# Optimization experiments

Measured on AMD Instinct MI355X. Metric: run time of the kernel, lower is better.

## Reference

```python
import jax, jax.numpy as jnp
import numpy as np

SIGMA = 1.0
DELTA = 1.0
TOPK = 10
TOPK_HALF = 5  # int(np.around(TOPK / 2))


def l2norm(x):
    # F.normalize: x / max(||x||, 1e-12)
    n = jnp.linalg.norm(x, axis=-1, keepdims=True)
    return x / jnp.maximum(n, 1e-12)


def cdist(a, b):
    # pairwise euclidean distance with grad-safe sqrt (0 on exact-zero dists)
    d2 = (jnp.sum(a * a, axis=1)[:, None] + jnp.sum(b * b, axis=1)[None, :]
          - 2.0 * a @ b.T)
    d2 = jnp.maximum(d2, 0.0)
    return jnp.where(d2 > 0.0, jnp.sqrt(jnp.where(d2 > 0.0, d2, 1.0)), 0.0)


def rc_weights(t_emb, idx):
    # all of this is under torch.no_grad() in the original
    N = t_emb.shape[0]
    T_dist = cdist(t_emb, t_emb)
    W_P = jnp.exp(-(T_dist ** 2) / SIGMA)
    same_id = idx[:, None] == idx[None, :]
    W_P_copy = jnp.where(same_id, 1.0, W_P)
    _, topk_index = jax.lax.top_k(W_P_copy, TOPK)            # [N, k]
    topk_half_index = topk_index[:, :TOPK_HALF]               # [N, k/2]
    rows = jnp.arange(N)[:, None]
    W_NN = jnp.zeros((N, N), W_P.dtype).at[rows, topk_index].set(1.0)
    V = (((W_NN + W_NN.T) / 2.0) == 1.0).astype(W_P.dtype)    # mutual-NN graph
    # vectorized form of the per-row loop:
    # W_C_tilda[i, j] = V[i, j] * |N(i) \cap N(j)| / |N(i)|
    deg = V.sum(axis=1)                                       # |N(i)| per row
    VV = V @ V                                                # V symmetric -> (V@V)[i,j] = |N(i) cap N(j)|
    W_C_tilda = jnp.where(V > 0.0, VV / jnp.maximum(deg, 1.0)[:, None], 0.0)
    W_C_hat = W_C_tilda[topk_half_index].mean(axis=1)         # [N, N]
    W_C = (W_C_hat + W_C_hat.T) / 2.0
    W = (W_P + W_C) / 2.0
    off_diag = 1.0 - jnp.eye(N, dtype=W.dtype)
    pos_weight = W * off_diag
    neg_weight = (1.0 - W) * off_diag
    return pos_weight, neg_weight


def rc_loss(s_emb, t_emb, idx):
    s_emb = l2norm(s_emb)        # disable_mu=True
    t_emb = l2norm(t_emb)
    N = s_emb.shape[0]
    S_dist = cdist(s_emb, s_emb)
    S_dist = S_dist / S_dist.mean(axis=1, keepdims=True)
    pos_w, neg_w = rc_weights(t_emb, idx)
    pos_w = jax.lax.stop_gradient(pos_w)
    neg_w = jax.lax.stop_gradient(neg_w)
    pull = jax.nn.relu(S_dist) ** 2 * pos_w
    push = jax.nn.relu(DELTA - S_dist) ** 2 * neg_w
    return (pull.sum() + push.sum()) / (N * (N - 1))


def kl_loss(s_f, s_g):
    # disable_mu=True -> normalize both
    s_f = l2norm(s_f)
    s_g = l2norm(s_g)
    N = s_f.shape[0]
    S_dist = cdist(s_f, s_f)
    S_dist = S_dist / S_dist.mean(axis=1, keepdims=True)
    S_bg = cdist(s_g, s_g)
    S_bg = S_bg / S_bg.mean(axis=1, keepdims=True)
    log_q = jax.nn.log_softmax(-S_dist, axis=-1)
    log_p = jax.nn.log_softmax(jax.lax.stop_gradient(-S_bg), axis=-1)
    p = jnp.exp(log_p)
    return jnp.sum(p * (log_p - log_q)) / N


def setup_inputs() -> dict:
    key = jax.random.key(0)
    k1, k2, k3, k4 = jax.random.split(key, 4)
    N = 4096
    s_f = jax.random.normal(k1, (N, 512), jnp.float32)
    s_g = jax.random.normal(k2, (N, 512), jnp.float32)
    t_g = jax.random.normal(k3, (N, 1024), jnp.float32)
    idx = jax.random.randint(k4, (N,), 0, 2048, jnp.int64 if jax.config.jax_enable_x64 else jnp.int32)
    return {"s_f": s_f, "s_g": s_g, "t_g": t_g, "idx": idx}


def reference(s_f, s_g, t_g, idx):
    loss_RC_f = rc_loss(s_f, t_g, idx)
    loss_RC_g = rc_loss(s_g, t_g, idx)
    loss_RC = (loss_RC_f + loss_RC_g) / 2.0
    loss_KL = kl_loss(s_f, s_g)
    return loss_RC, loss_KL, loss_RC + loss_KL
```

## Files before the change

### kernel.cpp

```cpp
#include <hip/hip_runtime.h>
#include <hip/hip_bf16.h>

#define NN 4096
typedef unsigned short u16;
typedef __bf16 bf16x8 __attribute__((ext_vector_type(8)));
typedef float f32x4 __attribute__((ext_vector_type(4)));
typedef u16 u16x8 __attribute__((ext_vector_type(8)));

typedef const __attribute__((address_space(1))) void* gptr_t;
typedef __attribute__((address_space(3))) void* lptr_t;

__device__ inline u16 bf16bits(float v) {
    __bf16 h = (__bf16)v;
    return __builtin_bit_cast(u16, h);
}
__device__ inline float bf16val(float v) {
    __bf16 h = (__bf16)v;
    return (float)h;
}
__device__ inline float b2f(u16 b) { return __uint_as_float(((unsigned)b) << 16); }

__device__ inline float block_sum(float v, volatile float* sbuf) {
    int lane = threadIdx.x & 63, wv = threadIdx.x >> 6;
#pragma unroll
    for (int o = 32; o > 0; o >>= 1) v += __shfl_xor(v, o, 64);
    if (lane == 0) sbuf[wv] = v;
    __syncthreads();
    float r = sbuf[0] + sbuf[1] + sbuf[2] + sbuf[3];
    __syncthreads();
    return r;
}

template <int D>
__global__ void normalize_kernel(const float* __restrict__ in, u16* __restrict__ outb,
                                 float* __restrict__ ssout) {
    __shared__ float sbuf[4];
    constexpr int NV = D / 4;
    int row = blockIdx.x, tid = threadIdx.x;
    const float4* x4 = (const float4*)(in + (size_t)row * D);
    float4 v = make_float4(0.f, 0.f, 0.f, 0.f);
    if (tid < NV) v = x4[tid];
    float s = v.x * v.x + v.y * v.y + v.z * v.z + v.w * v.w;
    float tot = block_sum(s, sbuf);
    float inv = 1.0f / fmaxf(sqrtf(tot), 1e-12f);
    float sb = 0.f;
    if (tid < NV) {
        float b0 = bf16val(v.x * inv), b1 = bf16val(v.y * inv);
        float b2 = bf16val(v.z * inv), b3 = bf16val(v.w * inv);
        ushort4 o;
        o.x = bf16bits(v.x * inv);
        o.y = bf16bits(v.y * inv);
        o.z = bf16bits(v.z * inv);
        o.w = bf16bits(v.w * inv);
        ((ushort4*)(outb + (size_t)row * D))[tid] = o;
        sb = b0 * b0 + b1 * b1 + b2 * b2 + b3 * b3;
    }
    float totb = block_sum(sb, sbuf);
    if (tid == 0) ssout[row] = totb;
}

#define TS 132
__launch_bounds__(256)
__global__ void gram_merged(const u16* __restrict__ tb, const u16* __restrict__ fb,
                            const u16* __restrict__ gb, const float* __restrict__ ss_t,
                            const float* __restrict__ ss_f, const float* __restrict__ ss_g,
                            u16* __restrict__ WP, u16* __restrict__ Sf, u16* __restrict__ Sg,
                            float* __restrict__ rsf, float* __restrict__ rsg) {
    __shared__ __align__(16) u16 smem[24576];

    int bid = blockIdx.x;
    int seg = (bid < 528) ? 0 : (bid < 1056 ? 1 : 2);
    int p = bid - seg * 528;
    int l = (p & 7) * 66 + (p >> 3);
    int by = 0, rem = l;
    while (rem >= 32 - by) { rem -= 32 - by; ++by; }
    int bx = by + rem;

    const u16* X = (seg == 0) ? tb : (seg == 1 ? fb : gb);
    const float* ss = (seg == 0) ? ss_t : (seg == 1 ? ss_f : ss_g);
    u16* outp = (seg == 0) ? WP : (seg == 1 ? Sf : Sg);
    float* rowsum = (seg == 0) ? nullptr : (seg == 1 ? rsf : rsg);
    const int K = (seg == 0) ? 1024 : 512;
    const bool mode1 = (seg != 0);
    const bool offdiag = (bx != by);

    const int tid = threadIdx.x;
    const int wv = tid >> 6, lane = tid & 63;
    const int wr = wv >> 1, wc = wv & 1;
    const int brow = by * 128, bcol = bx * 128;
    const int r = lane & 15, kc = lane >> 4;
    const int crow = lane >> 2;
    const int koff = (lane & 3) * 8;

    f32x4 acc[4][4];
#pragma unroll
    for (int mi = 0; mi < 4; ++mi)
#pragma unroll
        for (int ni = 0; ni < 4; ++ni) acc[mi][ni] = (f32x4){0.f, 0.f, 0.f, 0.f};

    auto STAGE = [&](int buf, int k0) {
#pragma unroll
        for (int cc = 0; cc < 2; ++cc) {
            int c = wv * 2 + cc;
            const u16* ga = X + (size_t)(brow + c * 16 + crow) * K + k0 + koff;
            const u16* gbp = X + (size_t)(bcol + c * 16 + crow) * K + k0 + koff;
            __builtin_amdgcn_global_load_lds((gptr_t)ga, (lptr_t)&smem[buf * 4096 + c * 512], 16, 0, 0);
            __builtin_amdgcn_global_load_lds((gptr_t)gbp, (lptr_t)&smem[12288 + buf * 4096 + c * 512], 16, 0, 0);
        }
    };

    const int NT = K / 32;
    STAGE(0, 0);
    STAGE(1, 32);
    for (int t = 0; t < NT; ++t) {
        int cur = t % 3;
        if (t == NT - 1) asm volatile("s_waitcnt vmcnt(0)" ::: "memory");
        else             asm volatile("s_waitcnt vmcnt(4)" ::: "memory");
        __builtin_amdgcn_sched_barrier(0);
        __builtin_amdgcn_s_barrier();

        bf16x8 af[4], bfr[4];
#pragma unroll
        for (int mi = 0; mi < 4; ++mi)
            af[mi] = *(const bf16x8*)&smem[cur * 4096 + (wr * 64 + mi * 16 + r) * 32 + kc * 8];
#pragma unroll
        for (int ni = 0; ni < 4; ++ni)
            bfr[ni] = *(const bf16x8*)&smem[12288 + cur * 4096 + (wc * 64 + ni * 16 + r) * 32 + kc * 8];

        if (t + 2 < NT) STAGE((t + 2) % 3, (t + 2) * 32);

        asm volatile("s_waitcnt lgkmcnt(0)" ::: "memory");
        __builtin_amdgcn_sched_barrier(0);
        __builtin_amdgcn_s_barrier();

#pragma unroll
        for (int mi = 0; mi < 4; ++mi)
#pragma unroll
            for (int ni = 0; ni < 4; ++ni)
                acc[mi][ni] = __builtin_amdgcn_mfma_f32_16x16x32_bf16(af[mi], bfr[ni], acc[mi][ni], 0, 0, 0);
    }
    __syncthreads();

    u16* tile = smem;
    const int q = lane >> 4;
#pragma unroll
    for (int mi = 0; mi < 4; ++mi) {
#pragma unroll
        for (int v = 0; v < 4; ++v) {
            int rl = wr * 64 + mi * 16 + q * 4 + v;
            float ssi = ss[brow + rl];
#pragma unroll
            for (int ni = 0; ni < 4; ++ni) {
                int cl = wc * 64 + ni * 16 + r;
                float d2 = fmaxf(ssi + ss[bcol + cl] - 2.0f * acc[mi][ni][v], 0.f);
                float o = mode1 ? sqrtf(d2) : __expf(-d2);
                tile[rl * TS + cl] = bf16bits(o);
            }
        }
    }
    __syncthreads();

    {
        int rl = tid >> 1, hf = tid & 1;
        const u16* srow = &tile[rl * TS + hf * 64];
        u16* drow = outp + (size_t)(brow + rl) * NN + bcol + hf * 64;
        float rs = 0.f;
#pragma unroll
        for (int i = 0; i < 8; ++i) {
            ushort4 aa = *(const ushort4*)(srow + i * 8);
            ushort4 bb = *(const ushort4*)(srow + i * 8 + 4);
            u16x8 pk = {aa.x, aa.y, aa.z, aa.w, bb.x, bb.y, bb.z, bb.w};
            *(u16x8*)(drow + i * 8) = pk;
            if (mode1)
                rs += b2f(aa.x) + b2f(aa.y) + b2f(aa.z) + b2f(aa.w) +
                      b2f(bb.x) + b2f(bb.y) + b2f(bb.z) + b2f(bb.w);
        }
        if (mode1) {
            rs += __shfl_xor(rs, 1, 64);
            if (hf == 0) atomicAdd(&rowsum[brow + rl], rs);
        }
    }

    if (offdiag) {
        int c = tid >> 1, hf = tid & 1;
        u16* drow = outp + (size_t)(bcol + c) * NN + brow + hf * 64;
        float rs = 0.f;
#pragma unroll
        for (int s = 0; s < 8; ++s) {
            u16 g[8];
#pragma unroll
            for (int u = 0; u < 8; ++u) g[u] = tile[(hf * 64 + s * 8 + u) * TS + c];
            u16x8 pk = {g[0], g[1], g[2], g[3], g[4], g[5], g[6], g[7]};
            *(u16x8*)(drow + s * 8) = pk;
            if (mode1)
#pragma unroll
                for (int u = 0; u < 8; ++u) rs += b2f(g[u]);
        }
        if (mode1) {
            rs += __shfl_xor(rs, 1, 64);
            if (hf == 0) atomicAdd(&rowsum[bcol + c], rs);
        }
    }
}

__global__ void topk_kernel(const u16* __restrict__ WP, const int* __restrict__ idx,
                            int* __restrict__ topk) {
    __shared__ unsigned long long sred[4];
    __shared__ unsigned long long sbest;
    int row = blockIdx.x, tid = threadIdx.x;
    int myid = idx[row];
    const u16x8* W8 = (const u16x8*)(WP + (size_t)row * NN);
    const int4* idx4 = (const int4*)idx;
    unsigned key[16];
#pragma unroll
    for (int a = 0; a < 2; ++a) {
        u16x8 w = W8[a * 256 + tid];
        int4 iA = idx4[a * 512 + tid * 2];
        int4 iB = idx4[a * 512 + tid * 2 + 1];
        int ids[8] = {iA.x, iA.y, iA.z, iA.w, iB.x, iB.y, iB.z, iB.w};
#pragma unroll
        for (int c = 0; c < 8; ++c)
            key[a * 8 + c] = (ids[c] == myid) ? 0x3F800000u : (((unsigned)w[c]) << 16);
    }
    int lane = tid & 63, wv = tid >> 6;
    for (int it = 0; it < 10; ++it) {
        unsigned long long best = 0;
#pragma unroll
        for (int a = 0; a < 2; ++a)
#pragma unroll
            for (int c = 0; c < 8; ++c) {
                unsigned j = (unsigned)(a * 2048 + tid * 8 + c);
                unsigned long long pk =
                    ((unsigned long long)key[a * 8 + c] << 32) | (0xFFFFFFFFu - j);
                if (pk > best) best = pk;
            }
#pragma unroll
        for (int o = 32; o > 0; o >>= 1) {
            unsigned long long t = __shfl_xor(best, o, 64);
            if (t > best) best = t;
        }
        if (lane == 0) sred[wv] = best;
        __syncthreads();
        if (tid == 0) {
            unsigned long long b = sred[0];
            for (int w2 = 1; w2 < 4; ++w2)
                if (sred[w2] > b) b = sred[w2];
            sbest = b;
        }
        __syncthreads();
        unsigned jstar = 0xFFFFFFFFu - (unsigned)(sbest & 0xFFFFFFFFu);
        if (tid == 0) topk[row * 10 + it] = (int)jstar;
        if (((jstar >> 3) & 255u) == (unsigned)tid) {
            unsigned slot = ((jstar >> 11) << 3) | (jstar & 7u);
#pragma unroll
            for (int a = 0; a < 16; ++a)
                if ((unsigned)a == slot) key[a] = 0u;
        }
        __syncthreads();
    }
}

__global__ void mutual_kernel(const int* __restrict__ topk, int* __restrict__ nbr,
                              int* __restrict__ deg) {
    int gid = blockIdx.x * 256 + threadIdx.x;
    if (gid >= NN * 10) return;
    int i = gid / 10, a = gid - i * 10;
    int j = topk[i * 10 + a];
    bool mut = false;
#pragma unroll
    for (int b = 0; b < 10; ++b) mut = mut || (topk[j * 10 + b] == i);
    nbr[gid] = mut ? j : -1;
    if (mut) atomicAdd(&deg[i], 1);
}

__global__ void tilda_kernel(const int* __restrict__ nbr, const int* __restrict__ deg,
                             float* __restrict__ tvals) {
    int gid = blockIdx.x * 256 + threadIdx.x;
    if (gid >= NN * 10) return;
    int m = gid / 10;
    int j = nbr[gid];
    if (j < 0) { tvals[gid] = 0.f; return; }
    int am[10], aj[10];
#pragma unroll
    for (int p = 0; p < 10; ++p) am[p] = nbr[m * 10 + p];
#pragma unroll
    for (int p = 0; p < 10; ++p) aj[p] = nbr[j * 10 + p];
    int cnt = 0;
#pragma unroll
    for (int p = 0; p < 10; ++p)
#pragma unroll
        for (int qq = 0; qq < 10; ++qq)
            cnt += (am[p] >= 0 && am[p] == aj[qq]) ? 1 : 0;
    int dm = deg[m];
    float dv = (float)(dm > 1 ? dm : 1);
    tvals[gid] = (float)cnt / dv;
}

__global__ void hat_kernel(const int* __restrict__ topk, const int* __restrict__ nbr,
                           const float* __restrict__ tvals, int* __restrict__ hcols,
                           float* __restrict__ hvals) {
    int gid = blockIdx.x * 256 + threadIdx.x;
    if (gid >= NN * 5) return;
    int i = gid / 5, h = gid - i * 5;
    int m = topk[i * 10 + h];
#pragma unroll
    for (int a = 0; a < 10; ++a) {
        int j = nbr[m * 10 + a];
        int slot = i * 50 + h * 10 + a;
        hcols[slot] = j;
        hvals[slot] = (j >= 0) ? tvals[m * 10 + a] * 0.2f : 0.f;
    }
}

__global__ void fused_dense_kernel(const u16* __restrict__ Sf, const u16* __restrict__ Sg,
                                   const u16* __restrict__ WP, const float* __restrict__ rsf,
                                   const float* __restrict__ rsg, double* __restrict__ acc) {
    __shared__ float sbuf[4];
    int row = blockIdx.x, tid = threadIdx.x;
    float imf = (float)NN / rsf[row];
    float img = (float)NN / rsg[row];
    const u16x8* f8 = (const u16x8*)(Sf + (size_t)row * NN);
    const u16x8* g8 = (const u16x8*)(Sg + (size_t)row * NN);
    const u16x8* w8 = (const u16x8*)(WP + (size_t)row * NN);
    u16x8 fr[2], gr[2];
#pragma unroll
    for (int a = 0; a < 2; ++a) {
        fr[a] = f8[a * 256 + tid];
        gr[a] = g8[a * 256 + tid];
    }
    float vf[16], vg[16];
#pragma unroll
    for (int a = 0; a < 2; ++a)
#pragma unroll
        for (int c = 0; c < 8; ++c) {
            vf[a * 8 + c] = b2f(fr[a][c]) * imf;
            vg[a * 8 + c] = b2f(gr[a][c]) * img;
        }
    float ef = 0.f, eg = 0.f;
#pragma unroll
    for (int a = 0; a < 16; ++a) {
        ef += __expf(-vf[a]);
        eg += __expf(-vg[a]);
    }
    float lf = logf(block_sum(ef, sbuf));
    float lg = logf(block_sum(eg, sbuf));
    u16x8 wr2[2];
#pragma unroll
    for (int a = 0; a < 2; ++a) wr2[a] = w8[a * 256 + tid];
    float af = 0.f, ag = 0.f, akl = 0.f;
#pragma unroll
    for (int a = 0; a < 2; ++a) {
#pragma unroll
        for (int c = 0; c < 8; ++c) {
            int j = a * 2048 + tid * 8 + c;
            float wp = b2f(wr2[a][c]);
            float sf = vf[a * 8 + c], sg = vg[a * 8 + c];
            if (j != row) {
                float t = fmaxf(1.f - sf, 0.f);
                float pu = t * t;
                float gq = sf * sf - pu;
                af += pu + 0.5f * gq * wp;
                t = fmaxf(1.f - sg, 0.f);
                pu = t * t;
                gq = sg * sg - pu;
                ag += pu + 0.5f * gq * wp;
            }
            float lq = -sf - lf;
            float lp = -sg - lg;
            float pp = __expf(lp);
            akl += pp * (lp - lq);
        }
    }
    float tf = block_sum(af, sbuf);
    float tg2 = block_sum(ag, sbuf);
    float tk = block_sum(akl, sbuf);
    if (tid == 0) {
        int bank = (row & 15) * 3;
        atomicAdd(&acc[bank + 0], (double)tf);
        atomicAdd(&acc[bank + 1], (double)tg2);
        atomicAdd(&acc[bank + 2], (double)tk);
    }
}

__global__ void sparse_kernel(const u16* __restrict__ Sf, const u16* __restrict__ Sg,
                              const int* __restrict__ hcols, const float* __restrict__ hvals,
                              const float* __restrict__ rsf, const float* __restrict__ rsg,
                              double* __restrict__ acc) {
    __shared__ float sbuf[4];
    int lane = threadIdx.x & 63, wv = threadIdx.x >> 6;
    int i = blockIdx.x * 4 + wv;
    float cf = 0.f, cg = 0.f;
    if (lane < 50) {
        int j = hcols[i * 50 + lane];
        if (j >= 0 && j != i) {
            float v = hvals[i * 50 + lane];
            float imfi = (float)NN / rsf[i];
            float imgi = (float)NN / rsg[i];
            float s1 = b2f(Sf[(size_t)i * NN + j]) * imfi;
            float s2 = b2f(Sf[(size_t)j * NN + i]) * ((float)NN / rsf[j]);
            float t1 = fmaxf(1.f - s1, 0.f), t2 = fmaxf(1.f - s2, 0.f);
            cf = v * ((s1 * s1 - t1 * t1) + (s2 * s2 - t2 * t2));
            s1 = b2f(Sg[(size_t)i * NN + j]) * imgi;
            s2 = b2f(Sg[(size_t)j * NN + i]) * ((float)NN / rsg[j]);
            t1 = fmaxf(1.f - s1, 0.f);
            t2 = fmaxf(1.f - s2, 0.f);
            cg = v * ((s1 * s1 - t1 * t1) + (s2 * s2 - t2 * t2));
        }
    }
    float tf = block_sum(cf, sbuf);
    float tg = block_sum(cg, sbuf);
    if (threadIdx.x == 0) {
        int bank = (blockIdx.x & 15) * 3;
        atomicAdd(&acc[bank + 0], (double)(0.25f * tf));
        atomicAdd(&acc[bank + 1], (double)(0.25f * tg));
    }
}

__global__ void finalize_kernel(const double* __restrict__ acc, float* __restrict__ out) {
    if (threadIdx.x == 0) {
        double a0 = 0.0, a1 = 0.0, a2 = 0.0;
        for (int b = 0; b < 16; ++b) {
            a0 += acc[b * 3 + 0];
            a1 += acc[b * 3 + 1];
            a2 += acc[b * 3 + 2];
        }
        double denom = (double)NN * (double)(NN - 1);
        double rcf = a0 / denom, rcg = a1 / denom;
        double rc = 0.5 * (rcf + rcg);
        double kl = a2 / (double)NN;
        out[0] = (float)rc;
        out[1] = (float)kl;
        out[2] = (float)(rc + kl);
    }
}

extern "C" void kernel_launch(void* const* d_in, const int* in_sizes, int n_in, void* d_out,
                              int out_size, void* d_ws, size_t ws_size, hipStream_t stream) {
    const float* s_f = (const float*)d_in[0];
    const float* s_g = (const float*)d_in[1];
    const float* t_g = (const float*)d_in[2];
    const int* idx = (const int*)d_in[3];
    float* out = (float*)d_out;

    char* base = (char*)d_ws;
    size_t off = 0;
    auto alloc = [&](size_t b) {
        char* p = base + off;
        off = (off + b + 255) & ~(size_t)255;
        return p;
    };
    double* acc = (double*)alloc(16 * 3 * 8);
    float* rowsum_f = (float*)alloc(NN * 4);
    float* rowsum_g = (float*)alloc(NN * 4);
    int* deg = (int*)alloc(NN * 4);
    size_t zero_bytes = off;
    u16* tb = (u16*)alloc((size_t)NN * 1024 * 2);
    u16* fb = (u16*)alloc((size_t)NN * 512 * 2);
    u16* gb = (u16*)alloc((size_t)NN * 512 * 2);
    float* ss_t = (float*)alloc(NN * 4);
    float* ss_f = (float*)alloc(NN * 4);
    float* ss_g = (float*)alloc(NN * 4);
    u16* WP = (u16*)alloc((size_t)NN * NN * 2);
    u16* Sf = (u16*)alloc((size_t)NN * NN * 2);
    u16* Sg = (u16*)alloc((size_t)NN * NN * 2);
    int* topk = (int*)alloc(NN * 10 * 4);
    int* nbr = (int*)alloc(NN * 10 * 4);
    float* tvals = (float*)alloc(NN * 10 * 4);
    int* hcols = (int*)alloc(NN * 50 * 4);
    float* hvals = (float*)alloc(NN * 50 * 4);

    hipMemsetAsync(d_ws, 0, zero_bytes, stream);

    normalize_kernel<1024><<<NN, 256, 0, stream>>>(t_g, tb, ss_t);
    normalize_kernel<512><<<NN, 256, 0, stream>>>(s_f, fb, ss_f);
    normalize_kernel<512><<<NN, 256, 0, stream>>>(s_g, gb, ss_g);

    gram_merged<<<1584, 256, 0, stream>>>(tb, fb, gb, ss_t, ss_f, ss_g, WP, Sf, Sg,
                                          rowsum_f, rowsum_g);

    topk_kernel<<<NN, 256, 0, stream>>>(WP, idx, topk);
    mutual_kernel<<<(NN * 10 + 255) / 256, 256, 0, stream>>>(topk, nbr, deg);
    tilda_kernel<<<(NN * 10 + 255) / 256, 256, 0, stream>>>(nbr, deg, tvals);
    hat_kernel<<<(NN * 5 + 255) / 256, 256, 0, stream>>>(topk, nbr, tvals, hcols, hvals);

    fused_dense_kernel<<<NN, 256, 0, stream>>>(Sf, Sg, WP, rowsum_f, rowsum_g, acc);
    sparse_kernel<<<NN / 4, 256, 0, stream>>>(Sf, Sg, hcols, hvals, rowsum_f, rowsum_g, acc);
    finalize_kernel<<<1, 64, 0, stream>>>(acc, out);
}
```

Baseline: 229.1 us.

## Compute distance row sums in dense kernel, drop gram atomics and extra barrier

The per-row sums of the S_f/S_g distance matrices move out of the gram epilogue, where they were built from bf16 conversions and float atomics on both the tile and its transposed copy. They are now computed inside fused_dense_kernel, which already loads each full row, and written out for sparse_kernel to reuse. The second s_barrier per K-step in the gram main loop is removed; a sched_barrier is added after the first barrier instead. The double accumulator banks are spread over 64 slots with a stride of 8 to reduce atomic contention. The cost is an extra block reduction per row in the dense kernel, and the loop relies on the triple-buffer ordering to stay race-free without the second barrier.

```diff
diff --git a/kernel.cpp b/kernel.cpp
--- a/kernel.cpp
+++ b/kernel.cpp
@@ -64,8 +64,7 @@
 __global__ void gram_merged(const u16* __restrict__ tb, const u16* __restrict__ fb,
                             const u16* __restrict__ gb, const float* __restrict__ ss_t,
                             const float* __restrict__ ss_f, const float* __restrict__ ss_g,
-                            u16* __restrict__ WP, u16* __restrict__ Sf, u16* __restrict__ Sg,
-                            float* __restrict__ rsf, float* __restrict__ rsg) {
+                            u16* __restrict__ WP, u16* __restrict__ Sf, u16* __restrict__ Sg) {
     __shared__ __align__(16) u16 smem[24576];
 
     int bid = blockIdx.x;
@@ -79,7 +78,6 @@
     const u16* X = (seg == 0) ? tb : (seg == 1 ? fb : gb);
     const float* ss = (seg == 0) ? ss_t : (seg == 1 ? ss_f : ss_g);
     u16* outp = (seg == 0) ? WP : (seg == 1 ? Sf : Sg);
-    float* rowsum = (seg == 0) ? nullptr : (seg == 1 ? rsf : rsg);
     const int K = (seg == 0) ? 1024 : 512;
     const bool mode1 = (seg != 0);
     const bool offdiag = (bx != by);
@@ -118,6 +116,7 @@
         else             asm volatile("s_waitcnt vmcnt(4)" ::: "memory");
         __builtin_amdgcn_sched_barrier(0);
         __builtin_amdgcn_s_barrier();
+        __builtin_amdgcn_sched_barrier(0);
 
         bf16x8 af[4], bfr[4];
 #pragma unroll
@@ -131,7 +130,6 @@
 
         asm volatile("s_waitcnt lgkmcnt(0)" ::: "memory");
         __builtin_amdgcn_sched_barrier(0);
-        __builtin_amdgcn_s_barrier();
 
 #pragma unroll
         for (int mi = 0; mi < 4; ++mi)
@@ -164,27 +162,18 @@
         int rl = tid >> 1, hf = tid & 1;
         const u16* srow = &tile[rl * TS + hf * 64];
         u16* drow = outp + (size_t)(brow + rl) * NN + bcol + hf * 64;
-        float rs = 0.f;
 #pragma unroll
         for (int i = 0; i < 8; ++i) {
             ushort4 aa = *(const ushort4*)(srow + i * 8);
             ushort4 bb = *(const ushort4*)(srow + i * 8 + 4);
             u16x8 pk = {aa.x, aa.y, aa.z, aa.w, bb.x, bb.y, bb.z, bb.w};
             *(u16x8*)(drow + i * 8) = pk;
-            if (mode1)
-                rs += b2f(aa.x) + b2f(aa.y) + b2f(aa.z) + b2f(aa.w) +
-                      b2f(bb.x) + b2f(bb.y) + b2f(bb.z) + b2f(bb.w);
-        }
-        if (mode1) {
-            rs += __shfl_xor(rs, 1, 64);
-            if (hf == 0) atomicAdd(&rowsum[brow + rl], rs);
         }
     }
 
     if (offdiag) {
         int c = tid >> 1, hf = tid & 1;
         u16* drow = outp + (size_t)(bcol + c) * NN + brow + hf * 64;
-        float rs = 0.f;
 #pragma unroll
         for (int s = 0; s < 8; ++s) {
             u16 g[8];
@@ -192,13 +181,6 @@
             for (int u = 0; u < 8; ++u) g[u] = tile[(hf * 64 + s * 8 + u) * TS + c];
             u16x8 pk = {g[0], g[1], g[2], g[3], g[4], g[5], g[6], g[7]};
             *(u16x8*)(drow + s * 8) = pk;
-            if (mode1)
-#pragma unroll
-                for (int u = 0; u < 8; ++u) rs += b2f(g[u]);
-        }
-        if (mode1) {
-            rs += __shfl_xor(rs, 1, 64);
-            if (hf == 0) atomicAdd(&rowsum[bcol + c], rs);
         }
     }
 }
@@ -313,12 +295,10 @@
 }
 
 __global__ void fused_dense_kernel(const u16* __restrict__ Sf, const u16* __restrict__ Sg,
-                                   const u16* __restrict__ WP, const float* __restrict__ rsf,
-                                   const float* __restrict__ rsg, double* __restrict__ acc) {
+                                   const u16* __restrict__ WP, float* __restrict__ rsf,
+                                   float* __restrict__ rsg, double* __restrict__ acc) {
     __shared__ float sbuf[4];
     int row = blockIdx.x, tid = threadIdx.x;
-    float imf = (float)NN / rsf[row];
-    float img = (float)NN / rsg[row];
     const u16x8* f8 = (const u16x8*)(Sf + (size_t)row * NN);
     const u16x8* g8 = (const u16x8*)(Sg + (size_t)row * NN);
     const u16x8* w8 = (const u16x8*)(WP + (size_t)row * NN);
@@ -328,6 +308,22 @@
         fr[a] = f8[a * 256 + tid];
         gr[a] = g8[a * 256 + tid];
     }
+    float sf_ = 0.f, sg_ = 0.f;
+#pragma unroll
+    for (int a = 0; a < 2; ++a)
+#pragma unroll
+        for (int c = 0; c < 8; ++c) {
+            sf_ += b2f(fr[a][c]);
+            sg_ += b2f(gr[a][c]);
+        }
+    float rsum_f = block_sum(sf_, sbuf);
+    float rsum_g = block_sum(sg_, sbuf);
+    if (tid == 0) {
+        rsf[row] = rsum_f;
+        rsg[row] = rsum_g;
+    }
+    float imf = (float)NN / rsum_f;
+    float img = (float)NN / rsum_g;
     float vf[16], vg[16];
 #pragma unroll
     for (int a = 0; a < 2; ++a)
@@ -375,7 +371,7 @@
     float tg2 = block_sum(ag, sbuf);
     float tk = block_sum(akl, sbuf);
     if (tid == 0) {
-        int bank = (row & 15) * 3;
+        int bank = (row & 63) * 8;
         atomicAdd(&acc[bank + 0], (double)tf);
         atomicAdd(&acc[bank + 1], (double)tg2);
         atomicAdd(&acc[bank + 2], (double)tk);
@@ -410,7 +406,7 @@
     float tf = block_sum(cf, sbuf);
     float tg = block_sum(cg, sbuf);
     if (threadIdx.x == 0) {
-        int bank = (blockIdx.x & 15) * 3;
+        int bank = (blockIdx.x & 63) * 8;
         atomicAdd(&acc[bank + 0], (double)(0.25f * tf));
         atomicAdd(&acc[bank + 1], (double)(0.25f * tg));
     }
@@ -419,10 +415,10 @@
 __global__ void finalize_kernel(const double* __restrict__ acc, float* __restrict__ out) {
     if (threadIdx.x == 0) {
         double a0 = 0.0, a1 = 0.0, a2 = 0.0;
-        for (int b = 0; b < 16; ++b) {
-            a0 += acc[b * 3 + 0];
-            a1 += acc[b * 3 + 1];
-            a2 += acc[b * 3 + 2];
+        for (int b = 0; b < 64; ++b) {
+            a0 += acc[b * 8 + 0];
+            a1 += acc[b * 8 + 1];
+            a2 += acc[b * 8 + 2];
         }
         double denom = (double)NN * (double)(NN - 1);
         double rcf = a0 / denom, rcg = a1 / denom;
@@ -449,11 +445,11 @@
         off = (off + b + 255) & ~(size_t)255;
         return p;
     };
-    double* acc = (double*)alloc(16 * 3 * 8);
+    double* acc = (double*)alloc(64 * 8 * 8);
+    int* deg = (int*)alloc(NN * 4);
+    size_t zero_bytes = off;
     float* rowsum_f = (float*)alloc(NN * 4);
     float* rowsum_g = (float*)alloc(NN * 4);
-    int* deg = (int*)alloc(NN * 4);
-    size_t zero_bytes = off;
     u16* tb = (u16*)alloc((size_t)NN * 1024 * 2);
     u16* fb = (u16*)alloc((size_t)NN * 512 * 2);
     u16* gb = (u16*)alloc((size_t)NN * 512 * 2);
@@ -475,8 +471,7 @@
     normalize_kernel<512><<<NN, 256, 0, stream>>>(s_f, fb, ss_f);
     normalize_kernel<512><<<NN, 256, 0, stream>>>(s_g, gb, ss_g);
 
-    gram_merged<<<1584, 256, 0, stream>>>(tb, fb, gb, ss_t, ss_f, ss_g, WP, Sf, Sg,
-                                          rowsum_f, rowsum_g);
+    gram_merged<<<1584, 256, 0, stream>>>(tb, fb, gb, ss_t, ss_f, ss_g, WP, Sf, Sg);
 
     topk_kernel<<<NN, 256, 0, stream>>>(WP, idx, topk);
     mutual_kernel<<<(NN * 10 + 255) / 256, 256, 0, stream>>>(topk, nbr, deg);
```

Result: faster. 194.7 us (-15.0%).
